# Kernel optimization log

Hardware: AMD Instinct MI355X
Metric: run time of the kernel (lower is better)

Reference implementation:

```python
import jax, jax.numpy as jnp
import numpy as np


def _relative_position_index(ws: int) -> np.ndarray:
    # Matches torch meshgrid (ij) construction in _init_relative_positions.
    coords = np.stack(np.meshgrid(np.arange(ws), np.arange(ws), indexing='ij'), axis=0).reshape(2, -1)  # [2, ws*ws]
    rel = coords[:, :, None] - coords[:, None, :]          # [2, N, N]
    rel = rel.transpose(1, 2, 0).copy()                    # [N, N, 2]
    rel[:, :, 0] += ws - 1
    rel[:, :, 1] += ws - 1
    rel[:, :, 0] *= 2 * ws - 1
    return rel.sum(-1)                                     # [N, N] int


def setup_inputs() -> dict:
    key = jax.random.key(0)
    ks = jax.random.split(key, 6)
    B, N, C, H, WS = 4096, 49, 512, 16, 7
    x = jax.random.normal(ks[0], (B, N, C), dtype=jnp.float32)
    w_qkv = jax.random.normal(ks[1], (C, 3 * C), dtype=jnp.float32) * (C ** -0.5)
    b_qkv = jax.random.normal(ks[2], (3 * C,), dtype=jnp.float32) * 0.02
    w_proj = jax.random.normal(ks[3], (C, C), dtype=jnp.float32) * (C ** -0.5)
    b_proj = jax.random.normal(ks[4], (C,), dtype=jnp.float32) * 0.02
    bias_table = jax.random.normal(ks[5], ((2 * WS - 1) ** 2, H), dtype=jnp.float32) * 0.02
    return {"x": x, "w_qkv": w_qkv, "b_qkv": b_qkv, "w_proj": w_proj,
            "b_proj": b_proj, "bias_table": bias_table,
            "num_heads": H, "window_size": WS}


def reference(x, w_qkv, b_qkv, w_proj, b_proj, bias_table, num_heads, window_size):
    B, N, C = x.shape
    hd = C // num_heads
    qkv = (x @ w_qkv + b_qkv).reshape(B, N, 3, num_heads, hd)
    q, k, v = (qkv[:, :, i].transpose(0, 2, 1, 3) for i in range(3))  # each [B, H, N, hd]
    # NOTE: scale uses full channel dim C (as in source), not head_dim.
    attn = jnp.einsum('bhnd,bhmd->bhnm', q, k) * (C ** -0.5)          # [B, H, N, N]
    idx = _relative_position_index(window_size)                        # [N, N] static
    rel_bias = bias_table[idx].transpose(2, 0, 1)                      # [H, N, N]
    attn = jax.nn.softmax(attn + rel_bias[None], axis=-1)
    out = jnp.einsum('bhnm,bhmd->bhnd', attn, v)                       # [B, H, N, hd]
    out = out.transpose(0, 2, 1, 3).reshape(B, N, C)
    return out @ w_proj + b_proj
```

## Files before the change

kernel.cpp:

```cpp
#include <hip/hip_runtime.h>
#include <hip/hip_bf16.h>

typedef __attribute__((ext_vector_type(8))) short bf16x8;
typedef __attribute__((ext_vector_type(4))) float f32x4;

#define DEVI __device__ __forceinline__

DEVI short f2bf(float f) {
  union { float f; unsigned u; } v; v.f = f;
  unsigned r = v.u + 0x7FFFu + ((v.u >> 16) & 1u);
  return (short)(r >> 16);
}

DEVI void gl16(const void* g, void* l) {
  __builtin_amdgcn_global_load_lds((const __attribute__((address_space(1))) unsigned*)g,
                                   (__attribute__((address_space(3))) unsigned*)l,
                                   16, 0, 0);
}

DEVI float exp2a(float x) { float r; asm("v_exp_f32 %0, %1" : "=v"(r) : "v"(x)); return r; }

DEVI unsigned pk2(float lo, float hi) {
  union { __hip_bfloat162 h; unsigned u; } v;
  float2 f; f.x = lo; f.y = hi;
  v.h = __float22bfloat162_rn(f);
  return v.u;
}

union U8 { unsigned u[4]; bf16x8 v; };
DEVI bf16x8 mk8(unsigned a, unsigned b, unsigned c, unsigned d) {
  U8 x; x.u[0]=a; x.u[1]=b; x.u[2]=c; x.u[3]=d; return x.v;
}


__global__ __launch_bounds__(256) void conv_x_k(const float* __restrict__ x,
                                                short* __restrict__ xb) {
  long i = (long)blockIdx.x * 256 + threadIdx.x;
  const float4* xf = (const float4*)x;
  float4 a = xf[i * 2], c = xf[i * 2 + 1];
  bf16x8 r;
  r[0] = f2bf(a.x); r[1] = f2bf(a.y); r[2] = f2bf(a.z); r[3] = f2bf(a.w);
  r[4] = f2bf(c.x); r[5] = f2bf(c.y); r[6] = f2bf(c.z); r[7] = f2bf(c.w);
  *(bf16x8*)(xb + i * 8) = r;
}

__global__ __launch_bounds__(256) void conv_wT_k(const float* __restrict__ w,
                                                 short* __restrict__ wT, int Ncols) {
  int i = blockIdx.x * 256 + threadIdx.x;
  if (i >= Ncols * 512) return;
  int n = i >> 9, k = i & 511;
  wT[i] = f2bf(w[k * Ncols + n]);
}

__global__ __launch_bounds__(256) void fill_biasT(const float* __restrict__ btab,
                                                  float* __restrict__ biasT) {
  int i = blockIdx.x * 256 + threadIdx.x;
  int h = i >> 12, m = (i >> 6) & 63, n = i & 63;
  float v;
  if (m >= 49) {
    v = -1e30f;
  } else {
    int nn = n > 48 ? 48 : n;
    int ni = nn / 7, nj = nn - ni * 7;
    int mi = m / 7,  mj = m - mi * 7;
    int idx = (ni - mi + 6) * 13 + (nj - mj + 6);
    v = btab[idx * 16 + h] * 1.4426950408889634f;
  }
  biasT[i] = v;
}


template <int EPI>
__global__ __launch_bounds__(512, 2)
void gemm256(const short* __restrict__ A, const short* __restrict__ Bt,
             const float* __restrict__ bias, void* __restrict__ outp, int ctiles) {
  __shared__ short Ls[65536];

  const int nwg = gridDim.x;
  const int w = blockIdx.x;
  const int chunk = nwg >> 3;
  const int tid = (w & 7) * chunk + (w >> 3);
  const int rt = tid / ctiles, ct = tid % ctiles;
  const long m0 = (long)rt * 256;
  const int n0 = ct * 256;

  const int t = threadIdx.x;
  const int lane = t & 63;
  const int wv = t >> 6;
  const int wr = wv >> 2;
  const int wc = wv & 3;
  const int l15 = lane & 15, g = lane >> 4;

  const int gch = (t & 3) ^ ((t >> 3) & 3);
  const short* Ag = A + (m0 + (t >> 2)) * 512 + gch * 8;
  const short* Bg = Bt + (long)(n0 + (t >> 2)) * 512 + gch * 8;

  const int cA = ((g ^ ((l15 >> 1) & 3))) * 8;
  const int rowA = (wr * 128 + l15) * 32;
  const int rowB = (wc * 64 + l15) * 32;

  f32x4 acc[8][4] = {};
  bf16x8 af[8], bfr[2];

#define STAGE_A(ktn, kh, bufn)                                         \
  { const short* s_ = Ag + (ktn) * 64 + (kh) * 32;                     \
    short* d_ = (bufn) + (kh) * 8192 + t * 8;                          \
    gl16(s_, d_); gl16(s_ + 128 * 512, d_ + 4096); }
#define STAGE_B(ktn, kh, bufn)                                         \
  { const short* s_ = Bg + (ktn) * 64 + (kh) * 32;                     \
    short* d_ = (bufn) + 16384 + (kh) * 8192 + t * 8;                  \
    gl16(s_, d_); gl16(s_ + 128 * 512, d_ + 4096); }
#define LOAD_AF(Ab, kh)                                                \
  _Pragma("unroll")                                                    \
  for (int mf = 0; mf < 8; ++mf)                                       \
    af[mf] = *(const bf16x8*)((Ab) + (kh) * 8192 + rowA + mf * 512 + cA);
#define LOAD_BF(Ab, kh, nh)                                            \
  bfr[0] = *(const bf16x8*)((Ab) + 16384 + (kh) * 8192 + rowB + ((nh) * 2) * 512 + cA); \
  bfr[1] = *(const bf16x8*)((Ab) + 16384 + (kh) * 8192 + rowB + ((nh) * 2 + 1) * 512 + cA);
#define MFMA16(nh)                                                     \
  __builtin_amdgcn_s_setprio(1);                                       \
  _Pragma("unroll")                                                    \
  for (int mf = 0; mf < 8; ++mf) {                                     \
    acc[mf][(nh) * 2] = __builtin_amdgcn_mfma_f32_16x16x32_bf16(af[mf], bfr[0], acc[mf][(nh) * 2], 0, 0, 0);         \
    acc[mf][(nh) * 2 + 1] = __builtin_amdgcn_mfma_f32_16x16x32_bf16(af[mf], bfr[1], acc[mf][(nh) * 2 + 1], 0, 0, 0); \
  }                                                                    \
  __builtin_amdgcn_s_setprio(0);
#define BAR() asm volatile("s_barrier" ::: "memory")
#define VMW4() asm volatile("s_waitcnt vmcnt(4)" ::: "memory")

  STAGE_A(0, 0, Ls); STAGE_B(0, 0, Ls); STAGE_A(0, 1, Ls); STAGE_B(0, 1, Ls);
  VMW4();
  BAR();

  for (int kt = 0; kt < 8; ++kt) {
    const short* Ab = Ls + (kt & 1) * 32768;
    short* Bn = Ls + ((kt & 1) ^ 1) * 32768;
    const int ktn = kt < 7 ? kt + 1 : 7;

    LOAD_AF(Ab, 0); LOAD_BF(Ab, 0, 0);
    STAGE_A(ktn, 0, Bn);
    BAR(); MFMA16(0); BAR();

    LOAD_BF(Ab, 0, 1);
    STAGE_B(ktn, 0, Bn);
    VMW4();
    BAR(); MFMA16(1); BAR();

    LOAD_AF(Ab, 1); LOAD_BF(Ab, 1, 0);
    STAGE_A(ktn, 1, Bn);
    BAR(); MFMA16(0); BAR();

    LOAD_BF(Ab, 1, 1);
    STAGE_B(ktn, 1, Bn);
    VMW4();
    BAR(); MFMA16(1); BAR();
  }

  if (EPI == 0) {
    short* qkv = (short*)outp;
#pragma unroll
    for (int mf = 0; mf < 8; ++mf)
#pragma unroll
      for (int r = 0; r < 4; ++r) {
        int row = (int)m0 + wr * 128 + mf * 16 + g * 4 + r;
        int b = row / 49, n = row - b * 49;
#pragma unroll
        for (int nf = 0; nf < 4; ++nf) {
          int col = n0 + wc * 64 + nf * 16 + l15;
          float val = acc[mf][nf][r] + bias[col];
          int ii = col >> 9, h = (col >> 5) & 15, d = col & 31;
          qkv[(long)((b * 16 + h) * 3 + ii) * 1568 + n * 32 + d] = f2bf(val);
        }
      }
  } else {
    float* out = (float*)outp;
#pragma unroll
    for (int mf = 0; mf < 8; ++mf)
#pragma unroll
      for (int r = 0; r < 4; ++r) {
        long row = m0 + wr * 128 + mf * 16 + g * 4 + r;
#pragma unroll
        for (int nf = 0; nf < 4; ++nf) {
          int col = n0 + wc * 64 + nf * 16 + l15;
          out[row * 512 + col] = acc[mf][nf][r] + bias[col];
        }
      }
  }
#undef STAGE_A
#undef STAGE_B
#undef LOAD_AF
#undef LOAD_BF
#undef MFMA16
#undef BAR
#undef VMW4
}


__global__ __launch_bounds__(256, 3)
void attn49(const short* __restrict__ qkvb, const float* __restrict__ biasT,
            short* __restrict__ ao) {
  const int t = threadIdx.x, lane = t & 63, wv = t >> 6;
  const int l15 = lane & 15, g = lane >> 4, g4 = g * 4;
  const int b = blockIdx.x >> 2;
  const int h = (blockIdx.x & 3) * 4 + wv;

  const short* qb = qkvb + (long)(b * 16 + h) * 3 * 1568;
  const short* kb = qb + 1568;
  const short* vb = kb + 1568;

  bf16x8 qf[4], kf[4];
#pragma unroll
  for (int i = 0; i < 4; ++i) {
    int row = i * 16 + l15; row = row > 48 ? 48 : row;
    kf[i] = *(const bf16x8*)(kb + row * 32 + g * 8);
    qf[i] = *(const bf16x8*)(qb + row * 32 + g * 8);
  }

  bf16x8 vf[2][2];
#pragma unroll
  for (int kt = 0; kt < 2; ++kt)
#pragma unroll
    for (int hi = 0; hi < 2; ++hi)
#pragma unroll
      for (int r = 0; r < 4; ++r) {
        int m = kt * 32 + hi * 16 + g4 + r;
        m = m > 48 ? 48 : m;
#pragma unroll
        for (int dt = 0; dt < 2; ++dt)
          vf[kt][dt][hi * 4 + r] = vb[m * 32 + dt * 16 + l15];
      }

  f32x4 s[4][4] = {};
#pragma unroll
  for (int i = 0; i < 4; ++i)
#pragma unroll
    for (int j = 0; j < 4; ++j)
      s[i][j] = __builtin_amdgcn_mfma_f32_16x16x32_bf16(kf[i], qf[j], s[i][j], 0, 0, 0);

  const float* biasH = biasT + h * 4096;
  float sum[4] = {0.f, 0.f, 0.f, 0.f};
#pragma unroll
  for (int i = 0; i < 4; ++i)
#pragma unroll
    for (int r = 0; r < 4; ++r) {
      int m = i * 16 + g4 + r;
      const float* bp = biasH + m * 64 + l15;
#pragma unroll
      for (int j = 0; j < 4; ++j) {
        float p = exp2a(fmaf(s[i][j][r], 0.06375871f, bp[j * 16]));
        s[i][j][r] = p;
        sum[j] += p;
      }
    }
#pragma unroll
  for (int j = 0; j < 4; ++j) {
    sum[j] += __shfl_xor(sum[j], 16);
    sum[j] += __shfl_xor(sum[j], 32);
    sum[j] = 1.f / sum[j];
  }

  unsigned pk[4][4][2];
#pragma unroll
  for (int j = 0; j < 4; ++j)
#pragma unroll
    for (int i = 0; i < 4; ++i) {
      pk[j][i][0] = pk2(s[i][j][0] * sum[j], s[i][j][1] * sum[j]);
      pk[j][i][1] = pk2(s[i][j][2] * sum[j], s[i][j][3] * sum[j]);
    }

  f32x4 o[4][2] = {};
#pragma unroll
  for (int j = 0; j < 4; ++j) {
    bf16x8 a0 = mk8(pk[j][0][0], pk[j][0][1], pk[j][1][0], pk[j][1][1]);
    bf16x8 a1 = mk8(pk[j][2][0], pk[j][2][1], pk[j][3][0], pk[j][3][1]);
    o[j][0] = __builtin_amdgcn_mfma_f32_16x16x32_bf16(a0, vf[0][0], o[j][0], 0, 0, 0);
    o[j][0] = __builtin_amdgcn_mfma_f32_16x16x32_bf16(a1, vf[1][0], o[j][0], 0, 0, 0);
    o[j][1] = __builtin_amdgcn_mfma_f32_16x16x32_bf16(a0, vf[0][1], o[j][1], 0, 0, 0);
    o[j][1] = __builtin_amdgcn_mfma_f32_16x16x32_bf16(a1, vf[1][1], o[j][1], 0, 0, 0);
  }

#pragma unroll
  for (int j = 0; j < 4; ++j)
#pragma unroll
    for (int r = 0; r < 4; ++r) {
      int n = j * 16 + g4 + r;
      if (n < 49) {
        long off = ((long)b * 49 + n) * 512 + h * 32 + l15;
        ao[off]      = f2bf(o[j][0][r]);
        ao[off + 16] = f2bf(o[j][1][r]);
      }
    }
}


extern "C" void kernel_launch(void* const* d_in, const int* in_sizes, int n_in,
                              void* d_out, int out_size, void* d_ws, size_t ws_size,
                              hipStream_t stream) {
  (void)in_sizes; (void)n_in; (void)out_size; (void)ws_size;
  const float* x      = (const float*)d_in[0];
  const float* w_qkv  = (const float*)d_in[1];
  const float* b_qkv  = (const float*)d_in[2];
  const float* w_proj = (const float*)d_in[3];
  const float* b_proj = (const float*)d_in[4];
  const float* btab   = (const float*)d_in[5];

  char* ws = (char*)d_ws;
  short* xb  = (short*)ws;
  short* wqT = (short*)(ws + 205520896L);
  short* wpT = (short*)(ws + 205520896L + 1572864L);
  short* qkv = (short*)(ws + 205520896L + 1572864L + 524288L);
  short* ao  = xb;
  float* biasT = (float*)wqT;

  conv_x_k <<<50176, 256, 0, stream>>>(x, xb);
  conv_wT_k<<<3072, 256, 0, stream>>>(w_qkv, wqT, 1536);
  conv_wT_k<<<1024, 256, 0, stream>>>(w_proj, wpT, 512);
  gemm256<0><<<4704, 512, 0, stream>>>(xb, wqT, b_qkv, (void*)qkv, 6);
  fill_biasT<<<256, 256, 0, stream>>>(btab, biasT);
  attn49   <<<16384, 256, 0, stream>>>(qkv, biasT, ao);
  gemm256<1><<<1568, 512, 0, stream>>>(ao, wpT, b_proj, d_out, 2);
}
```

Measured before the change: 895.2 us.

## Stage QKV epilogue through LDS, cache V in LDS, merge prep kernels

The QKV GEMM epilogue now writes bf16 results into shared memory and then stores them to the head-major QKV layout as 16-byte vectors, replacing scattered 2-byte global stores. The attention kernel copies each head's V block into shared memory and gathers the transposed V fragments from there rather than from global memory, and it issues the QK MFMAs before that gather. The two weight-transpose kernels and the bias-table fill are merged into one launch, and biasT is moved into the tail of the output buffer so the fill can run before the QKV GEMM. The trade-offs are extra barriers and LDS traffic in the epilogue, and a dependence on the projection GEMM overwriting the bias scratch only after attention has finished reading it.

```diff
diff --git a/kernel.cpp b/kernel.cpp
--- a/kernel.cpp
+++ b/kernel.cpp
@@ -44,29 +44,36 @@
   *(bf16x8*)(xb + i * 8) = r;
 }
 
-__global__ __launch_bounds__(256) void conv_wT_k(const float* __restrict__ w,
-                                                 short* __restrict__ wT, int Ncols) {
-  int i = blockIdx.x * 256 + threadIdx.x;
-  if (i >= Ncols * 512) return;
-  int n = i >> 9, k = i & 511;
-  wT[i] = f2bf(w[k * Ncols + n]);
-}
-
-__global__ __launch_bounds__(256) void fill_biasT(const float* __restrict__ btab,
-                                                  float* __restrict__ biasT) {
-  int i = blockIdx.x * 256 + threadIdx.x;
-  int h = i >> 12, m = (i >> 6) & 63, n = i & 63;
-  float v;
-  if (m >= 49) {
-    v = -1e30f;
+__global__ __launch_bounds__(256) void prep_k(const float* __restrict__ wq,
+                                              const float* __restrict__ wp,
+                                              const float* __restrict__ btab,
+                                              short* __restrict__ wqT,
+                                              short* __restrict__ wpT,
+                                              float* __restrict__ biasT) {
+  int bid = blockIdx.x;
+  if (bid < 3072) {
+    int i = bid * 256 + threadIdx.x;
+    int n = i >> 9, k = i & 511;
+    wqT[i] = f2bf(wq[k * 1536 + n]);
+  } else if (bid < 4096) {
+    int i = (bid - 3072) * 256 + threadIdx.x;
+    int n = i >> 9, k = i & 511;
+    wpT[i] = f2bf(wp[k * 512 + n]);
   } else {
-    int nn = n > 48 ? 48 : n;
-    int ni = nn / 7, nj = nn - ni * 7;
-    int mi = m / 7,  mj = m - mi * 7;
-    int idx = (ni - mi + 6) * 13 + (nj - mj + 6);
-    v = btab[idx * 16 + h] * 1.4426950408889634f;
-  }
-  biasT[i] = v;
+    int i = (bid - 4096) * 256 + threadIdx.x;
+    int h = i >> 12, m = (i >> 6) & 63, n = i & 63;
+    float v;
+    if (m >= 49) {
+      v = -1e30f;
+    } else {
+      int nn = n > 48 ? 48 : n;
+      int ni = nn / 7, nj = nn - ni * 7;
+      int mi = m / 7,  mj = m - mi * 7;
+      int idx = (ni - mi + 6) * 13 + (nj - mj + 6);
+      v = btab[idx * 16 + h] * 1.4426950408889634f;
+    }
+    biasT[i] = v;
+  }
 }
 
 
@@ -89,7 +96,7 @@
   const int wv = t >> 6;
   const int wr = wv >> 2;
   const int wc = wv & 3;
-  const int l15 = lane & 15, g = lane >> 4;
+  const int l15 = lane & 15, g = lane >> 4, g4 = g * 4;
 
   const int gch = (t & 3) ^ ((t >> 3) & 3);
   const short* Ag = A + (m0 + (t >> 2)) * 512 + gch * 8;
@@ -157,28 +164,41 @@
   }
 
   if (EPI == 0) {
+    __syncthreads();
+#pragma unroll
+    for (int mf = 0; mf < 8; ++mf)
+#pragma unroll
+      for (int r = 0; r < 4; ++r) {
+        int lrow = wr * 128 + mf * 16 + g4 + r;
+#pragma unroll
+        for (int nf = 0; nf < 4; ++nf) {
+          int lcol = wc * 64 + nf * 16 + l15;
+          Ls[lrow * 256 + lcol] = f2bf(acc[mf][nf][r] + bias[n0 + lcol]);
+        }
+      }
+    __syncthreads();
     short* qkv = (short*)outp;
+    const int cq = n0 >> 8;
+    const int ii = cq >> 1;
+#pragma unroll
+    for (int s = 0; s < 16; ++s) {
+      int c = s * 512 + t;
+      int row = c >> 5, sub = c & 31;
+      int hl = sub >> 2, d0 = (sub & 3) * 8;
+      int rg = (int)m0 + row;
+      int b = rg / 49, n = rg - b * 49;
+      int h = (cq & 1) * 8 + hl;
+      long dst = (long)((b * 16 + h) * 3 + ii) * 1568 + n * 32 + d0;
+      *(bf16x8*)(qkv + dst) = *(const bf16x8*)(Ls + row * 256 + hl * 32 + d0);
+    }
+  } else {
+    __syncthreads();
+    float* out = (float*)outp;
 #pragma unroll
     for (int mf = 0; mf < 8; ++mf)
 #pragma unroll
       for (int r = 0; r < 4; ++r) {
-        int row = (int)m0 + wr * 128 + mf * 16 + g * 4 + r;
-        int b = row / 49, n = row - b * 49;
-#pragma unroll
-        for (int nf = 0; nf < 4; ++nf) {
-          int col = n0 + wc * 64 + nf * 16 + l15;
-          float val = acc[mf][nf][r] + bias[col];
-          int ii = col >> 9, h = (col >> 5) & 15, d = col & 31;
-          qkv[(long)((b * 16 + h) * 3 + ii) * 1568 + n * 32 + d] = f2bf(val);
-        }
-      }
-  } else {
-    float* out = (float*)outp;
-#pragma unroll
-    for (int mf = 0; mf < 8; ++mf)
-#pragma unroll
-      for (int r = 0; r < 4; ++r) {
-        long row = m0 + wr * 128 + mf * 16 + g * 4 + r;
+        long row = m0 + wr * 128 + mf * 16 + g4 + r;
 #pragma unroll
         for (int nf = 0; nf < 4; ++nf) {
           int col = n0 + wc * 64 + nf * 16 + l15;
@@ -199,6 +219,8 @@
 __global__ __launch_bounds__(256, 3)
 void attn49(const short* __restrict__ qkvb, const float* __restrict__ biasT,
             short* __restrict__ ao) {
+  __shared__ short Vl[4][2048];
+
   const int t = threadIdx.x, lane = t & 63, wv = t >> 6;
   const int l15 = lane & 15, g = lane >> 4, g4 = g * 4;
   const int b = blockIdx.x >> 2;
@@ -207,6 +229,13 @@
   const short* qb = qkvb + (long)(b * 16 + h) * 3 * 1568;
   const short* kb = qb + 1568;
   const short* vb = kb + 1568;
+  short* Vs = Vl[wv];
+
+#pragma unroll
+  for (int it = 0; it < 4; ++it) {
+    int c = it * 64 + lane; c = c > 195 ? 195 : c;
+    *(bf16x8*)(Vs + c * 8) = *(const bf16x8*)(vb + c * 8);
+  }
 
   bf16x8 qf[4], kf[4];
 #pragma unroll
@@ -216,6 +245,13 @@
     qf[i] = *(const bf16x8*)(qb + row * 32 + g * 8);
   }
 
+  f32x4 s[4][4] = {};
+#pragma unroll
+  for (int i = 0; i < 4; ++i)
+#pragma unroll
+    for (int j = 0; j < 4; ++j)
+      s[i][j] = __builtin_amdgcn_mfma_f32_16x16x32_bf16(kf[i], qf[j], s[i][j], 0, 0, 0);
+
   bf16x8 vf[2][2];
 #pragma unroll
   for (int kt = 0; kt < 2; ++kt)
@@ -227,15 +263,8 @@
         m = m > 48 ? 48 : m;
 #pragma unroll
         for (int dt = 0; dt < 2; ++dt)
-          vf[kt][dt][hi * 4 + r] = vb[m * 32 + dt * 16 + l15];
-      }
-
-  f32x4 s[4][4] = {};
-#pragma unroll
-  for (int i = 0; i < 4; ++i)
-#pragma unroll
-    for (int j = 0; j < 4; ++j)
-      s[i][j] = __builtin_amdgcn_mfma_f32_16x16x32_bf16(kf[i], qf[j], s[i][j], 0, 0, 0);
+          vf[kt][dt][hi * 4 + r] = Vs[m * 32 + dt * 16 + l15];
+      }
 
   const float* biasH = biasT + h * 4096;
   float sum[4] = {0.f, 0.f, 0.f, 0.f};
@@ -296,7 +325,7 @@
 extern "C" void kernel_launch(void* const* d_in, const int* in_sizes, int n_in,
                               void* d_out, int out_size, void* d_ws, size_t ws_size,
                               hipStream_t stream) {
-  (void)in_sizes; (void)n_in; (void)out_size; (void)ws_size;
+  (void)in_sizes; (void)n_in; (void)ws_size;
   const float* x      = (const float*)d_in[0];
   const float* w_qkv  = (const float*)d_in[1];
   const float* b_qkv  = (const float*)d_in[2];
@@ -310,13 +339,11 @@
   short* wpT = (short*)(ws + 205520896L + 1572864L);
   short* qkv = (short*)(ws + 205520896L + 1572864L + 524288L);
   short* ao  = xb;
-  float* biasT = (float*)wqT;
-
-  conv_x_k <<<50176, 256, 0, stream>>>(x, xb);
-  conv_wT_k<<<3072, 256, 0, stream>>>(w_qkv, wqT, 1536);
-  conv_wT_k<<<1024, 256, 0, stream>>>(w_proj, wpT, 512);
+  float* biasT = (float*)d_out + (out_size - 65536);
+
+  conv_x_k<<<50176, 256, 0, stream>>>(x, xb);
+  prep_k  <<<4352, 256, 0, stream>>>(w_qkv, w_proj, btab, wqT, wpT, biasT);
   gemm256<0><<<4704, 512, 0, stream>>>(xb, wqT, b_qkv, (void*)qkv, 6);
-  fill_biasT<<<256, 256, 0, stream>>>(btab, biasT);
-  attn49   <<<16384, 256, 0, stream>>>(qkv, biasT, ao);
+  attn49  <<<16384, 256, 0, stream>>>(qkv, biasT, ao);
   gemm256<1><<<1568, 512, 0, stream>>>(ao, wpT, b_proj, d_out, 2);
 }
```

Measured after the change: 881.4 us. About the same (-1.5%).
